# Kernel optimization log

Hardware: AMD Instinct MI355X
Metric: run time of the kernel (lower is better)

The kernel has to match this reference:

```python
import jax, jax.numpy as jnp
import numpy as np
from jax import lax

T, B, IN = 50, 1024, 405
H, NMEM, DMEM, R, NWAY = 200, 128, 40, 4, 5
GAMMA = 0.99


def setup_inputs() -> dict:
    key = jax.random.key(0)
    ks = jax.random.split(key, 11)
    s = lambda *sh: 0.05
    return {
        "x": jax.random.normal(ks[0], (T, B, IN), jnp.float32),
        "W_ih": jax.random.normal(ks[1], (4 * H, IN), jnp.float32) * 0.05,
        "W_hh": jax.random.normal(ks[2], (4 * H, H), jnp.float32) * 0.05,
        "b_ih": jax.random.normal(ks[3], (4 * H,), jnp.float32) * 0.05,
        "b_hh": jax.random.normal(ks[4], (4 * H,), jnp.float32) * 0.05,
        "Wk": jax.random.normal(ks[5], (R * DMEM, H), jnp.float32) * 0.05,
        "bk": jax.random.normal(ks[6], (R * DMEM,), jnp.float32) * 0.05,
        "Ws": jax.random.normal(ks[7], (R, H), jnp.float32) * 0.05,
        "bs": jax.random.normal(ks[8], (R,), jnp.float32) * 0.05,
        "Wo": jax.random.normal(ks[9], (NWAY, H + R * DMEM), jnp.float32) * 0.05,
        "bo": jax.random.normal(ks[10], (NWAY,), jnp.float32) * 0.05,
    }


def _ntm_forward(x, W_ih, W_hh, b_ih, b_hh, Wk, bk, Ws, bs, Wo, bo):
    sg = lax.stop_gradient
    batch_idx = jnp.arange(B)

    def step(carry, x_t):
        h, c, M, wr, wu, wlu = carry
        # LSTM cell (torch nn.LSTMCell gate order: i, f, g, o)
        gates = x_t @ W_ih.T + b_ih + h @ W_hh.T + b_hh
        i, f, g, o = jnp.split(gates, 4, axis=-1)
        c = jax.nn.sigmoid(f) * c + jax.nn.sigmoid(i) * jnp.tanh(g)
        h = jax.nn.sigmoid(o) * jnp.tanh(c)
        # zero out least-used memory row (data-level op in torch)
        idx = jnp.argmin(wu, axis=1)
        M = M.at[batch_idx, idx].set(0.0)
        # keys and interpolation gate
        k = jnp.tanh(h @ Wk.T + bk).reshape(B, R, DMEM)
        sigma = jax.nn.sigmoid(jnp.tanh(h @ Ws.T + bs)).reshape(B, R, 1)
        # write weights and memory write
        ww = sigma * wr + (1.0 - sigma) * wlu[:, None, :]  # [B,R,NMEM]
        M = M + jnp.einsum("brm,brd->bmd", ww, k)
        # cosine-similarity read addressing
        nk = jnp.linalg.norm(k, axis=2)   # [B,R]
        nM = jnp.linalg.norm(M, axis=2)   # [B,NMEM]
        K = jnp.einsum("brd,bmd->brm", k, M) / (nk[:, :, None] * nM[:, None, :])
        wr_new = jax.nn.softmax(K, axis=-1)  # softmax over memory slots
        r = jnp.einsum("brm,bmd->brd", wr_new, M).reshape(B, R * DMEM)
        # output head: Linear -> Sigmoid -> Softmax (as in torch source)
        logits = jnp.concatenate([h, r], axis=1) @ Wo.T + bo
        out = jax.nn.softmax(jax.nn.sigmoid(logits), axis=-1)
        # usage update (all detached in torch)
        wr_d = sg(wr_new)
        wu = GAMMA * wu + jnp.sum(wr_d + sg(ww), axis=1)
        kth = -lax.top_k(-wu, R)[0][:, -1]  # k-th smallest usage
        wlu = sg((wu <= kth[:, None]).astype(M.dtype))
        return (h, c, sg(M), wr_d, wu, wlu), out

    carry0 = (
        jnp.zeros((B, H), x.dtype),
        jnp.zeros((B, H), x.dtype),
        jnp.zeros((B, NMEM, DMEM), x.dtype),
        jnp.zeros((B, R, NMEM), x.dtype),
        jnp.zeros((B, NMEM), x.dtype),
        jnp.ones((B, NMEM), x.dtype),
    )
    _, y = lax.scan(step, carry0, x)
    return y  # [T, B, NWAY]


def reference(x, W_ih, W_hh, b_ih, b_hh, Wk, bk, Ws, bs, Wo, bo):
    return _ntm_forward(x, W_ih, W_hh, b_ih, b_hh, Wk, bk, Ws, bs, Wo, bo)
```

## Files before the change

kernel.cpp:

```cpp
#include <hip/hip_runtime.h>
#include <stdint.h>

#define TSTEPS 50
#define BATCH  1024
#define INDIM  405
#define KP     448
#define HDIM   200
#define G4H    800
#define NMEM   128
#define DMEM   40
#define DPAD   41
#define RH     4
#define RD     160
#define NWAY   5
#define GAMMA_ 0.99f
#define NG     4
#define WROWS  928

typedef __attribute__((ext_vector_type(8))) short short8;
typedef __attribute__((ext_vector_type(4))) float f32x4;

__device__ __forceinline__ float sigmoidf_(float x) {
    return 1.f / (1.f + __expf(-x));
}
__device__ __forceinline__ float ftanh(float x) {
    float e = __expf(2.f * x);
    return 1.f - 2.f / (e + 1.f);
}
__device__ __forceinline__ unsigned short f2bf(float f) {
    uint32_t u = __float_as_uint(f);
    uint32_t r = u + 0x7FFFu + ((u >> 16) & 1u);
    return (unsigned short)(r >> 16);
}
__device__ __forceinline__ float bf2f(unsigned short h) {
    return __uint_as_float(((uint32_t)h) << 16);
}

__global__ void transpose_weights(const float* __restrict__ W_hh,
                                  const float* __restrict__ Wk,
                                  float* __restrict__ WhhT,
                                  float* __restrict__ WkT) {
    int i = blockIdx.x * 256 + threadIdx.x;
    if (i < HDIM * G4H) {
        int j = i / G4H, o = i % G4H;
        WhhT[i] = W_hh[o * HDIM + j];
    } else if (i < HDIM * G4H + HDIM * RD) {
        int e = i - HDIM * G4H;
        int j = e / RD, rd = e % RD;
        WkT[e] = Wk[rd * HDIM + j];
    }
}

__global__ __launch_bounds__(256) void convert_A(const float* __restrict__ x,
                                                 unsigned short* __restrict__ Ahi,
                                                 unsigned short* __restrict__ Alo) {
    int c = blockIdx.x * 256 + threadIdx.x;
    int r = blockIdx.y;
    if (c >= KP) return;
    float v = (c < INDIM) ? x[(size_t)r * INDIM + c] : 0.f;
    unsigned short hi = f2bf(v);
    unsigned short lo = f2bf(v - bf2f(hi));
    size_t o = (size_t)r * KP + c;
    Ahi[o] = hi;
    Alo[o] = lo;
}

__global__ __launch_bounds__(256) void convert_W(const float* __restrict__ W_ih,
                                                 unsigned short* __restrict__ Wpk) {
    int c = blockIdx.x * 256 + threadIdx.x;
    int n = blockIdx.y;
    int sec = blockIdx.z;
    if (c >= KP) return;
    float v = (n < G4H && c < INDIM) ? W_ih[(size_t)n * INDIM + c] : 0.f;
    unsigned short hi = f2bf(v);
    size_t o = (size_t)sec * WROWS * KP + (size_t)n * KP + c;
    Wpk[o] = (sec == 0) ? hi : f2bf(v - bf2f(hi));
}

__global__ __launch_bounds__(256) void gx_gemm_mfma(
        const unsigned short* __restrict__ Ahi,
        const unsigned short* __restrict__ Alo,
        const unsigned short* __restrict__ Wpk,
        const float* __restrict__ b_ih, const float* __restrict__ b_hh,
        float* __restrict__ gx) {
    __shared__ unsigned short Alds[128 * 64];
    __shared__ unsigned short Blds[128 * 64];
    const int tid = threadIdx.x;
    const int wv = tid >> 6, ln = tid & 63;
    const int wr = wv >> 1, wc = wv & 1;
    const int n0 = blockIdx.x * 128;
    const int m0 = blockIdx.y * 128;

    f32x4 acc[4][4];
#pragma unroll
    for (int m = 0; m < 4; ++m)
#pragma unroll
        for (int n = 0; n < 4; ++n) acc[m][n] = (f32x4){0.f, 0.f, 0.f, 0.f};

    int erow[4], ecol[4];
#pragma unroll
    for (int i = 0; i < 4; ++i) {
        int e = (i * 4 + wv) * 512 + ln * 8;
        erow[i] = e >> 6;
        ecol[i] = e & 63;
    }

    const unsigned short* Whi = Wpk;
    const unsigned short* Wlo = Wpk + (size_t)WROWS * KP;

#pragma unroll 1
    for (int s = 0; s < 3; ++s) {
        const unsigned short* Ab = ((s == 2) ? Alo : Ahi) + (size_t)m0 * KP;
        const unsigned short* Bb = ((s == 1) ? Wlo : Whi) + (size_t)n0 * KP;

        short8 ar[4], br[4];
#pragma unroll
        for (int i = 0; i < 4; ++i) {
            ar[i] = *(const short8*)&Ab[(size_t)erow[i] * KP + ecol[i]];
            br[i] = *(const short8*)&Bb[(size_t)erow[i] * KP + ecol[i]];
        }

#pragma unroll 1
        for (int k0 = 0; k0 < KP; k0 += 64) {
            __syncthreads();
#pragma unroll
            for (int i = 0; i < 4; ++i) {
                int e = (i * 4 + wv) * 512 + ln * 8;
                *(short8*)&Alds[e] = ar[i];
                *(short8*)&Blds[e] = br[i];
            }
            __syncthreads();
            if (k0 + 64 < KP) {
#pragma unroll
                for (int i = 0; i < 4; ++i) {
                    ar[i] = *(const short8*)&Ab[(size_t)erow[i] * KP + k0 + 64 + ecol[i]];
                    br[i] = *(const short8*)&Bb[(size_t)erow[i] * KP + k0 + 64 + ecol[i]];
                }
            }
#pragma unroll
            for (int ks = 0; ks < 2; ++ks) {
                short8 af[4], bf[4];
                int kcol = ks * 32 + (ln >> 4) * 8;
#pragma unroll
                for (int m = 0; m < 4; ++m) {
                    int row = wr * 64 + m * 16 + (ln & 15);
                    af[m] = *(const short8*)&Alds[row * 64 + kcol];
                }
#pragma unroll
                for (int n = 0; n < 4; ++n) {
                    int row = wc * 64 + n * 16 + (ln & 15);
                    bf[n] = *(const short8*)&Blds[row * 64 + kcol];
                }
#pragma unroll
                for (int m = 0; m < 4; ++m)
#pragma unroll
                    for (int n = 0; n < 4; ++n)
                        acc[m][n] = __builtin_amdgcn_mfma_f32_16x16x32_bf16(
                            af[m], bf[n], acc[m][n], 0, 0, 0);
            }
        }
    }

#pragma unroll
    for (int n = 0; n < 4; ++n) {
        int col = n0 + wc * 64 + n * 16 + (ln & 15);
        if (col >= G4H) continue;
        float bias = b_ih[col] + b_hh[col];
#pragma unroll
        for (int m = 0; m < 4; ++m) {
#pragma unroll
            for (int j = 0; j < 4; ++j) {
                int row = m0 + wr * 64 + m * 16 + (ln >> 4) * 4 + j;
                gx[(size_t)row * G4H + col] = acc[m][n][j] + bias;
            }
        }
    }
}

__global__ __launch_bounds__(256) void gx_gemm(const float* __restrict__ x,
                                               const float* __restrict__ W_ih,
                                               const float* __restrict__ b_ih,
                                               const float* __restrict__ b_hh,
                                               float* __restrict__ gx) {
    const int BM = 128, BN = 80, BK = 16;
    __shared__ float As[BK][BM];
    __shared__ float Bs[BK][BN];
    int m0 = blockIdx.y * BM;
    int n0 = blockIdx.x * BN;
    int tid = threadIdx.x;
    int tm = tid >> 4, tn = tid & 15;
    float acc[8][5];
#pragma unroll
    for (int i = 0; i < 8; ++i)
#pragma unroll
        for (int j = 0; j < 5; ++j) acc[i][j] = 0.f;

    for (int k0 = 0; k0 < INDIM; k0 += BK) {
        {
            int row = tid >> 1, kk = (tid & 1) * 8;
            const float* ap = x + (size_t)(m0 + row) * INDIM + k0 + kk;
#pragma unroll
            for (int i = 0; i < 8; ++i)
                As[kk + i][row] = (k0 + kk + i < INDIM) ? ap[i] : 0.f;
        }
        if (tid < 160) {
            int col = tid >> 1, kk = (tid & 1) * 8;
            const float* bp = W_ih + (size_t)(n0 + col) * INDIM + k0 + kk;
#pragma unroll
            for (int i = 0; i < 8; ++i)
                Bs[kk + i][col] = (k0 + kk + i < INDIM) ? bp[i] : 0.f;
        }
        __syncthreads();
#pragma unroll
        for (int k = 0; k < BK; ++k) {
            float a[8], b[5];
#pragma unroll
            for (int i = 0; i < 8; ++i) a[i] = As[k][tm * 8 + i];
#pragma unroll
            for (int j = 0; j < 5; ++j) b[j] = Bs[k][tn * 5 + j];
#pragma unroll
            for (int i = 0; i < 8; ++i)
#pragma unroll
                for (int j = 0; j < 5; ++j) acc[i][j] += a[i] * b[j];
        }
        __syncthreads();
    }
#pragma unroll
    for (int j = 0; j < 5; ++j) {
        int n = n0 + tn * 5 + j;
        float bias = b_ih[n] + b_hh[n];
#pragma unroll
        for (int i = 0; i < 8; ++i) {
            int m = m0 + tm * 8 + i;
            gx[(size_t)m * G4H + n] = acc[i][j] + bias;
        }
    }
}

__global__ __launch_bounds__(1024) void ntm_scan(
        const float* __restrict__ gx,
        const float* __restrict__ WhhT,
        const float* __restrict__ WkT,
        const float* __restrict__ bk,
        const float* __restrict__ Wsm,
        const float* __restrict__ bs,
        const float* __restrict__ Wo,
        const float* __restrict__ bo,
        float* __restrict__ out) {
    __shared__ float sM[NG][NMEM][DPAD];
    __shared__ float sh[NG][HDIM];
    __shared__ float sgate[NG][G4H];
    __shared__ float spartK[NG][4][RD];
    __shared__ float spartS[NG][RH][4];
    __shared__ float swr[NG][RH][NMEM];
    __shared__ float sww[NG][RH][NMEM];
    __shared__ float sKs[NG][RH][NMEM];
    __shared__ float swu[NG][NMEM];
    __shared__ float swlu[NG][NMEM];
    __shared__ float sk[NG][RH][DMEM];
    __shared__ float sr[NG][RD];
    __shared__ float snk[NG][RH];
    __shared__ float ssig[NG][RH];
    __shared__ float snM[NG][NMEM];
    __shared__ float stmp[NG][NWAY];
    __shared__ int   sidx[NG];

    const int tid = threadIdx.x;
    const int b0  = blockIdx.x * NG;

    for (int e = tid; e < NG * NMEM * DPAD; e += 1024) ((float*)sM)[e] = 0.f;
    for (int e = tid; e < NG * HDIM; e += 1024) ((float*)sh)[e] = 0.f;
    for (int e = tid; e < NG * RH * NMEM; e += 1024) ((float*)swr)[e] = 0.f;
    for (int e = tid; e < NG * NMEM; e += 1024) { ((float*)swu)[e] = 0.f; ((float*)swlu)[e] = 1.f; }

    float c_reg = 0.f;
    float gxr0 = 0.f, gxr1 = 0.f, gxr2 = 0.f, gxr3 = 0.f;
    if (tid < G4H) {
        const float* gxp = gx + (size_t)b0 * G4H + tid;
        gxr0 = gxp[0]; gxr1 = gxp[G4H]; gxr2 = gxp[2 * G4H]; gxr3 = gxp[3 * G4H];
    }
    __syncthreads();

    for (int t = 0; t < TSTEPS; ++t) {
        if (tid < G4H) {
            const int o = tid;
            float acc0 = 0.f, acc1 = 0.f, acc2 = 0.f, acc3 = 0.f;
#pragma unroll 2
            for (int j = 0; j < HDIM; j += 4) {
                float4 h0 = *(const float4*)&sh[0][j];
                float4 h1 = *(const float4*)&sh[1][j];
                float4 h2 = *(const float4*)&sh[2][j];
                float4 h3 = *(const float4*)&sh[3][j];
                float w0 = WhhT[(j + 0) * G4H + o];
                float w1 = WhhT[(j + 1) * G4H + o];
                float w2 = WhhT[(j + 2) * G4H + o];
                float w3 = WhhT[(j + 3) * G4H + o];
                acc0 += w0 * h0.x + w1 * h0.y + w2 * h0.z + w3 * h0.w;
                acc1 += w0 * h1.x + w1 * h1.y + w2 * h1.z + w3 * h1.w;
                acc2 += w0 * h2.x + w1 * h2.y + w2 * h2.z + w3 * h2.w;
                acc3 += w0 * h3.x + w1 * h3.y + w2 * h3.z + w3 * h3.w;
            }
            sgate[0][o] = acc0 + gxr0;
            sgate[1][o] = acc1 + gxr1;
            sgate[2][o] = acc2 + gxr2;
            sgate[3][o] = acc3 + gxr3;
            if (t + 1 < TSTEPS) {
                const float* gxp = gx + ((size_t)(t + 1) * BATCH + b0) * G4H + o;
                gxr0 = gxp[0]; gxr1 = gxp[G4H]; gxr2 = gxp[2 * G4H]; gxr3 = gxp[3 * G4H];
            }
        }
        __syncthreads();

        if (tid < NG * HDIM) {
            int gg = tid / HDIM, j = tid - gg * HDIM;
            float ig = sigmoidf_(sgate[gg][j]);
            float fg = sigmoidf_(sgate[gg][j + HDIM]);
            float gv = ftanh(sgate[gg][j + 2 * HDIM]);
            float og = sigmoidf_(sgate[gg][j + 3 * HDIM]);
            c_reg = fg * c_reg + ig * gv;
            sh[gg][j] = og * ftanh(c_reg);
        }
        __syncthreads();

        if (tid < 640) {
            int col = tid % RD, c = tid / RD;
            int jb = 52 * c - ((c == 3) ? 4 : 0);
            int je = jb + ((c < 2) ? 52 : 48);
            float a0 = 0.f, a1 = 0.f, a2 = 0.f, a3 = 0.f;
            for (int j = jb; j < je; j += 4) {
                float4 h0 = *(const float4*)&sh[0][j];
                float4 h1 = *(const float4*)&sh[1][j];
                float4 h2 = *(const float4*)&sh[2][j];
                float4 h3 = *(const float4*)&sh[3][j];
                float w0 = WkT[(j + 0) * RD + col];
                float w1 = WkT[(j + 1) * RD + col];
                float w2 = WkT[(j + 2) * RD + col];
                float w3 = WkT[(j + 3) * RD + col];
                a0 += w0 * h0.x + w1 * h0.y + w2 * h0.z + w3 * h0.w;
                a1 += w0 * h1.x + w1 * h1.y + w2 * h1.z + w3 * h1.w;
                a2 += w0 * h2.x + w1 * h2.y + w2 * h2.z + w3 * h2.w;
                a3 += w0 * h3.x + w1 * h3.y + w2 * h3.z + w3 * h3.w;
            }
            spartK[0][c][col] = a0; spartK[1][c][col] = a1;
            spartK[2][c][col] = a2; spartK[3][c][col] = a3;
        } else if (tid < 704) {
            int v = tid - 640; int g = v >> 4, rc = v & 15, r = rc >> 2, c = rc & 3;
            float a = 0.f;
            for (int j = 50 * c; j < 50 * c + 50; ++j) a += sh[g][j] * Wsm[r * HDIM + j];
            spartS[g][r][c] = a;
        } else if (tid < 960) {
            int a = tid - 704; int g = a >> 6, ln = a & 63;
            float v0 = swu[g][ln], v1 = swu[g][ln + 64];
            bool p1 = (v1 < v0);
            float mv = p1 ? v1 : v0;
            int   mi = p1 ? ln + 64 : ln;
#pragma unroll
            for (int off = 32; off; off >>= 1) {
                float ov = __shfl_xor(mv, off);
                int   oi = __shfl_xor(mi, off);
                if (ov < mv || (ov == mv && oi < mi)) { mv = ov; mi = oi; }
            }
            if (ln == 0) sidx[g] = mi;
        }
        __syncthreads();

        if (tid < 640) {
            int g = tid / RD, col = tid % RD;
            float s = spartK[g][0][col] + spartK[g][1][col]
                    + spartK[g][2][col] + spartK[g][3][col] + bk[col];
            sk[g][col / DMEM][col % DMEM] = ftanh(s);
        } else if (tid < 656) {
            int v = tid - 640; int g = v >> 2, r = v & 3;
            float s = spartS[g][r][0] + spartS[g][r][1]
                    + spartS[g][r][2] + spartS[g][r][3] + bs[r];
            ssig[g][r] = sigmoidf_(ftanh(s));
        } else if (tid < 816) {
            int v = tid - 656; int g = v / DMEM, d = v % DMEM;
            sM[g][sidx[g]][d] = 0.f;
        }
        __syncthreads();

#pragma unroll
        for (int q = 0; q < 2; ++q) {
            int e = tid + q * 1024;
            int g = e >> 9, rm = e & 511, r = rm >> 7, m = rm & 127;
            sww[g][r][m] = ssig[g][r] * swr[g][r][m] + (1.f - ssig[g][r]) * swlu[g][m];
        }
        if (tid < 16) {
            int g = tid >> 2, r = tid & 3;
            float s = 0.f;
            for (int d = 0; d < DMEM; ++d) { float v = sk[g][r][d]; s += v * v; }
            snk[g][r] = sqrtf(s);
        }
        __syncthreads();

        {
            int g = tid >> 8, mh = tid & 255, m = mh >> 1, d0 = (mh & 1) * 20;
            float w0 = sww[g][0][m], w1 = sww[g][1][m], w2 = sww[g][2][m], w3 = sww[g][3][m];
            for (int d = d0; d < d0 + 20; ++d) {
                float add = w0 * sk[g][0][d] + w1 * sk[g][1][d]
                          + w2 * sk[g][2][d] + w3 * sk[g][3][d];
                sM[g][m][d] += add;
            }
        }
        __syncthreads();

        if (tid < 512) {
            int g = tid >> 7, m = tid & 127;
            float s = 0.f;
            for (int d = 0; d < DMEM; ++d) { float v = sM[g][m][d]; s += v * v; }
            snM[g][m] = sqrtf(s);
        }
        __syncthreads();

#pragma unroll
        for (int q = 0; q < 2; ++q) {
            int e = tid + q * 1024;
            int g = e >> 9, rm = e & 511, r = rm >> 7, m = rm & 127;
            float acc = 0.f;
            for (int d = 0; d < DMEM; ++d) acc += sk[g][r][d] * sM[g][m][d];
            sKs[g][r][m] = acc / (snk[g][r] * snM[g][m]);
        }
        __syncthreads();

        {
            int w = tid >> 6, ln = tid & 63, g = w >> 2, r = w & 3;
            float a = sKs[g][r][ln];
            float b = sKs[g][r][ln + 64];
            float mx = fmaxf(a, b);
#pragma unroll
            for (int off = 32; off; off >>= 1) mx = fmaxf(mx, __shfl_xor(mx, off));
            float ea = __expf(a - mx), eb = __expf(b - mx);
            float s = ea + eb;
#pragma unroll
            for (int off = 32; off; off >>= 1) s += __shfl_xor(s, off);
            float inv = 1.f / s;
            swr[g][r][ln]      = ea * inv;
            swr[g][r][ln + 64] = eb * inv;
        }
        __syncthreads();

        if (tid < 640) {
            int g = tid / RD, rd = tid % RD, r = rd / DMEM, d = rd % DMEM;
            float acc = 0.f;
            for (int m = 0; m < NMEM; ++m) acc += swr[g][r][m] * sM[g][m][d];
            sr[g][rd] = acc;
        } else {
            for (int e = tid - 640; e < 512; e += 384) {
                int g = e >> 7, m = e & 127;
                float wu = GAMMA_ * swu[g][m];
#pragma unroll
                for (int r = 0; r < RH; ++r) wu += swr[g][r][m] + sww[g][r][m];
                swu[g][m] = wu;
            }
        }
        __syncthreads();

        if (tid < 640) {
            int g = tid / RD, v = tid % RD, o = v >> 5, ln = v & 31;
            const float* wrow = Wo + o * (HDIM + RD);
            float acc = 0.f;
            for (int j = ln; j < HDIM; j += 32) acc += sh[g][j] * wrow[j];
            for (int d = ln; d < RD; d += 32) acc += sr[g][d] * wrow[HDIM + d];
#pragma unroll
            for (int off = 16; off; off >>= 1) acc += __shfl_xor(acc, off, 32);
            if (ln == 0) stmp[g][o] = acc + bo[o];
        } else if (tid < 896) {
            int a = tid - 640; int g = a >> 6, ln = a & 63;
            float o0 = swu[g][ln], o1 = swu[g][ln + 64];
            float v0 = o0, v1 = o1, kth = 0.f;
#pragma unroll
            for (int it = 0; it < RH; ++it) {
                bool p1 = (v1 < v0);
                float mv = p1 ? v1 : v0;
                int   mi = p1 ? ln + 64 : ln;
                for (int off = 32; off; off >>= 1) {
                    float ov = __shfl_xor(mv, off);
                    int   oi = __shfl_xor(mi, off);
                    if (ov < mv || (ov == mv && oi < mi)) { mv = ov; mi = oi; }
                }
                kth = mv;
                if (mi == ln) v0 = __builtin_inff();
                else if (mi == ln + 64) v1 = __builtin_inff();
            }
            swlu[g][ln]      = (o0 <= kth) ? 1.f : 0.f;
            swlu[g][ln + 64] = (o1 <= kth) ? 1.f : 0.f;
        }
        __syncthreads();

        if (tid < NG) {
            int g = tid;
            float v[NWAY], mx = -1e30f;
#pragma unroll
            for (int o = 0; o < NWAY; ++o) { v[o] = sigmoidf_(stmp[g][o]); mx = fmaxf(mx, v[o]); }
            float s = 0.f;
#pragma unroll
            for (int o = 0; o < NWAY; ++o) { v[o] = __expf(v[o] - mx); s += v[o]; }
            float inv = 1.f / s;
            float* op = out + ((size_t)t * BATCH + (b0 + g)) * NWAY;
#pragma unroll
            for (int o = 0; o < NWAY; ++o) op[o] = v[o] * inv;
        }
    }
}

extern "C" void kernel_launch(void* const* d_in, const int* in_sizes, int n_in,
                              void* d_out, int out_size, void* d_ws, size_t ws_size,
                              hipStream_t stream) {
    const float* x    = (const float*)d_in[0];
    const float* W_ih = (const float*)d_in[1];
    const float* W_hh = (const float*)d_in[2];
    const float* b_ih = (const float*)d_in[3];
    const float* b_hh = (const float*)d_in[4];
    const float* Wk   = (const float*)d_in[5];
    const float* bk   = (const float*)d_in[6];
    const float* Wsm  = (const float*)d_in[7];
    const float* bs   = (const float*)d_in[8];
    const float* Wo   = (const float*)d_in[9];
    const float* bo   = (const float*)d_in[10];
    float* out = (float*)d_out;

    const size_t gx_elems   = (size_t)TSTEPS * BATCH * G4H;
    const size_t whht_elems = (size_t)HDIM * G4H;
    const size_t wkt_elems  = (size_t)HDIM * RD;
    const size_t f32_elems  = gx_elems + whht_elems + wkt_elems;
    const size_t a_elems    = (size_t)TSTEPS * BATCH * KP;
    const size_t w_elems    = (size_t)2 * WROWS * KP;
    const size_t need_f32   = f32_elems * sizeof(float);
    const size_t need_mfma  = need_f32 + (2 * a_elems + w_elems) * sizeof(unsigned short);
    if (ws_size < need_f32) return;

    float* ws   = (float*)d_ws;
    float* gxb  = ws;
    float* WhhT = ws + gx_elems;
    float* WkT  = WhhT + whht_elems;

    int tr_elems = HDIM * G4H + HDIM * RD;
    transpose_weights<<<dim3((tr_elems + 255) / 256), dim3(256), 0, stream>>>(W_hh, Wk, WhhT, WkT);

    if (ws_size >= need_mfma) {
        unsigned short* Ahi = (unsigned short*)(WkT + wkt_elems);
        unsigned short* Alo = Ahi + a_elems;
        unsigned short* Wpk = Alo + a_elems;
        convert_A<<<dim3(2, TSTEPS * BATCH), dim3(256), 0, stream>>>(x, Ahi, Alo);
        convert_W<<<dim3(2, WROWS, 2), dim3(256), 0, stream>>>(W_ih, Wpk);
        gx_gemm_mfma<<<dim3(7, (TSTEPS * BATCH) / 128), dim3(256), 0, stream>>>(
            Ahi, Alo, Wpk, b_ih, b_hh, gxb);
    } else {
        gx_gemm<<<dim3(G4H / 80, (TSTEPS * BATCH) / 128), dim3(256), 0, stream>>>(
            x, W_ih, b_ih, b_hh, gxb);
    }

    ntm_scan<<<dim3(BATCH / NG), dim3(1024), 0, stream>>>(gxb, WhhT, WkT, bk, Wsm, bs, Wo, bo, out);
}
```

Measured before the change: 1.649 ms.

## Use bf16 MFMA with hi/lo split for recurrent and key GEMMs, fuse scan stages

Measured after the change: 1.672 ms. Within noise of the previous version (+1.4%).

```diff
diff --git a/kernel.cpp b/kernel.cpp
--- a/kernel.cpp
+++ b/kernel.cpp
@@ -5,11 +5,13 @@
 #define BATCH  1024
 #define INDIM  405
 #define KP     448
+#define KH     224
+#define HBS    232
 #define HDIM   200
 #define G4H    800
 #define NMEM   128
 #define DMEM   40
-#define DPAD   41
+#define DPAD   44
 #define RH     4
 #define RD     160
 #define NWAY   5
@@ -36,18 +38,20 @@
     return __uint_as_float(((uint32_t)h) << 16);
 }
 
-__global__ void transpose_weights(const float* __restrict__ W_hh,
-                                  const float* __restrict__ Wk,
-                                  float* __restrict__ WhhT,
-                                  float* __restrict__ WkT) {
+__global__ __launch_bounds__(256) void convert_rec(const float* __restrict__ W_hh,
+                                                   const float* __restrict__ Wk,
+                                                   unsigned short* __restrict__ Whh_bf,
+                                                   unsigned short* __restrict__ Wk_bf) {
     int i = blockIdx.x * 256 + threadIdx.x;
-    if (i < HDIM * G4H) {
-        int j = i / G4H, o = i % G4H;
-        WhhT[i] = W_hh[o * HDIM + j];
-    } else if (i < HDIM * G4H + HDIM * RD) {
-        int e = i - HDIM * G4H;
-        int j = e / RD, rd = e % RD;
-        WkT[e] = Wk[rd * HDIM + j];
+    const int whh_e = G4H * KH;
+    const int wk_e  = RD * KH;
+    if (i < whh_e) {
+        int o = i / KH, k = i % KH;
+        Whh_bf[i] = f2bf(k < HDIM ? W_hh[o * HDIM + k] : 0.f);
+    } else if (i < whh_e + wk_e) {
+        int e = i - whh_e;
+        int o = e / KH, k = e % KH;
+        Wk_bf[e] = f2bf(k < HDIM ? Wk[o * HDIM + k] : 0.f);
     }
 }
 
@@ -237,10 +241,10 @@
     }
 }
 
-__global__ __launch_bounds__(1024) void ntm_scan(
+__global__ __launch_bounds__(1024, 4) void ntm_scan(
         const float* __restrict__ gx,
-        const float* __restrict__ WhhT,
-        const float* __restrict__ WkT,
+        const unsigned short* __restrict__ Whh_bf,
+        const unsigned short* __restrict__ Wk_bf,
         const float* __restrict__ bk,
         const float* __restrict__ Wsm,
         const float* __restrict__ bs,
@@ -249,9 +253,9 @@
         float* __restrict__ out) {
     __shared__ float sM[NG][NMEM][DPAD];
     __shared__ float sh[NG][HDIM];
+    __shared__ unsigned short shbf_hi[16][HBS];
+    __shared__ unsigned short shbf_lo[16][HBS];
     __shared__ float sgate[NG][G4H];
-    __shared__ float spartK[NG][4][RD];
-    __shared__ float spartS[NG][RH][4];
     __shared__ float swr[NG][RH][NMEM];
     __shared__ float sww[NG][RH][NMEM];
     __shared__ float sKs[NG][RH][NMEM];
@@ -267,89 +271,99 @@
 
     const int tid = threadIdx.x;
     const int b0  = blockIdx.x * NG;
+    const int w   = tid >> 6, l = tid & 63;
+    const int lr  = l & 15, lc = l >> 4;
 
     for (int e = tid; e < NG * NMEM * DPAD; e += 1024) ((float*)sM)[e] = 0.f;
     for (int e = tid; e < NG * HDIM; e += 1024) ((float*)sh)[e] = 0.f;
+    for (int e = tid; e < 16 * HBS; e += 1024) { ((unsigned short*)shbf_hi)[e] = 0; ((unsigned short*)shbf_lo)[e] = 0; }
     for (int e = tid; e < NG * RH * NMEM; e += 1024) ((float*)swr)[e] = 0.f;
     for (int e = tid; e < NG * NMEM; e += 1024) { ((float*)swu)[e] = 0.f; ((float*)swlu)[e] = 1.f; }
 
     float c_reg = 0.f;
     float gxr0 = 0.f, gxr1 = 0.f, gxr2 = 0.f, gxr3 = 0.f;
+    int pg = 0, pj = 0;
     if (tid < G4H) {
-        const float* gxp = gx + (size_t)b0 * G4H + tid;
-        gxr0 = gxp[0]; gxr1 = gxp[G4H]; gxr2 = gxp[2 * G4H]; gxr3 = gxp[3 * G4H];
+        pg = tid / HDIM; pj = tid - pg * HDIM;
+        const float* gxp = gx + (size_t)(b0 + pg) * G4H + pj;
+        gxr0 = gxp[0]; gxr1 = gxp[HDIM]; gxr2 = gxp[2 * HDIM]; gxr3 = gxp[3 * HDIM];
     }
     __syncthreads();
 
     for (int t = 0; t < TSTEPS; ++t) {
+        {
+            short8 bh[7], bl[7];
+#pragma unroll
+            for (int kk = 0; kk < 7; ++kk) {
+                bh[kk] = *(const short8*)&shbf_hi[lr][kk * 32 + lc * 8];
+                bl[kk] = *(const short8*)&shbf_lo[lr][kk * 32 + lc * 8];
+            }
+            for (int tile = w; tile < 50; tile += 16) {
+                const unsigned short* ap = Whh_bf + (size_t)(tile * 16 + lr) * KH + lc * 8;
+                short8 af[7];
+#pragma unroll
+                for (int kk = 0; kk < 7; ++kk) af[kk] = *(const short8*)&ap[kk * 32];
+                f32x4 acc = (f32x4){0.f, 0.f, 0.f, 0.f};
+#pragma unroll
+                for (int kk = 0; kk < 7; ++kk)
+                    acc = __builtin_amdgcn_mfma_f32_16x16x32_bf16(af[kk], bh[kk], acc, 0, 0, 0);
+#pragma unroll
+                for (int kk = 0; kk < 7; ++kk)
+                    acc = __builtin_amdgcn_mfma_f32_16x16x32_bf16(af[kk], bl[kk], acc, 0, 0, 0);
+                if (lr < NG) {
+#pragma unroll
+                    for (int j = 0; j < 4; ++j)
+                        sgate[lr][tile * 16 + lc * 4 + j] = acc[j];
+                }
+            }
+        }
+        __syncthreads();
+
         if (tid < G4H) {
-            const int o = tid;
-            float acc0 = 0.f, acc1 = 0.f, acc2 = 0.f, acc3 = 0.f;
-#pragma unroll 2
-            for (int j = 0; j < HDIM; j += 4) {
-                float4 h0 = *(const float4*)&sh[0][j];
-                float4 h1 = *(const float4*)&sh[1][j];
-                float4 h2 = *(const float4*)&sh[2][j];
-                float4 h3 = *(const float4*)&sh[3][j];
-                float w0 = WhhT[(j + 0) * G4H + o];
-                float w1 = WhhT[(j + 1) * G4H + o];
-                float w2 = WhhT[(j + 2) * G4H + o];
-                float w3 = WhhT[(j + 3) * G4H + o];
-                acc0 += w0 * h0.x + w1 * h0.y + w2 * h0.z + w3 * h0.w;
-                acc1 += w0 * h1.x + w1 * h1.y + w2 * h1.z + w3 * h1.w;
-                acc2 += w0 * h2.x + w1 * h2.y + w2 * h2.z + w3 * h2.w;
-                acc3 += w0 * h3.x + w1 * h3.y + w2 * h3.z + w3 * h3.w;
-            }
-            sgate[0][o] = acc0 + gxr0;
-            sgate[1][o] = acc1 + gxr1;
-            sgate[2][o] = acc2 + gxr2;
-            sgate[3][o] = acc3 + gxr3;
+            float ig = sigmoidf_(sgate[pg][pj] + gxr0);
+            float fg = sigmoidf_(sgate[pg][pj + HDIM] + gxr1);
+            float gv = ftanh(sgate[pg][pj + 2 * HDIM] + gxr2);
+            float og = sigmoidf_(sgate[pg][pj + 3 * HDIM] + gxr3);
+            c_reg = fg * c_reg + ig * gv;
+            float h = og * ftanh(c_reg);
+            sh[pg][pj] = h;
+            unsigned short hi = f2bf(h);
+            shbf_hi[pg][pj] = hi;
+            shbf_lo[pg][pj] = f2bf(h - bf2f(hi));
             if (t + 1 < TSTEPS) {
-                const float* gxp = gx + ((size_t)(t + 1) * BATCH + b0) * G4H + o;
-                gxr0 = gxp[0]; gxr1 = gxp[G4H]; gxr2 = gxp[2 * G4H]; gxr3 = gxp[3 * G4H];
-            }
-        }
-        __syncthreads();
-
-        if (tid < NG * HDIM) {
-            int gg = tid / HDIM, j = tid - gg * HDIM;
-            float ig = sigmoidf_(sgate[gg][j]);
-            float fg = sigmoidf_(sgate[gg][j + HDIM]);
-            float gv = ftanh(sgate[gg][j + 2 * HDIM]);
-            float og = sigmoidf_(sgate[gg][j + 3 * HDIM]);
-            c_reg = fg * c_reg + ig * gv;
-            sh[gg][j] = og * ftanh(c_reg);
-        }
-        __syncthreads();
-
-        if (tid < 640) {
-            int col = tid % RD, c = tid / RD;
-            int jb = 52 * c - ((c == 3) ? 4 : 0);
-            int je = jb + ((c < 2) ? 52 : 48);
-            float a0 = 0.f, a1 = 0.f, a2 = 0.f, a3 = 0.f;
-            for (int j = jb; j < je; j += 4) {
-                float4 h0 = *(const float4*)&sh[0][j];
-                float4 h1 = *(const float4*)&sh[1][j];
-                float4 h2 = *(const float4*)&sh[2][j];
-                float4 h3 = *(const float4*)&sh[3][j];
-                float w0 = WkT[(j + 0) * RD + col];
-                float w1 = WkT[(j + 1) * RD + col];
-                float w2 = WkT[(j + 2) * RD + col];
-                float w3 = WkT[(j + 3) * RD + col];
-                a0 += w0 * h0.x + w1 * h0.y + w2 * h0.z + w3 * h0.w;
-                a1 += w0 * h1.x + w1 * h1.y + w2 * h1.z + w3 * h1.w;
-                a2 += w0 * h2.x + w1 * h2.y + w2 * h2.z + w3 * h2.w;
-                a3 += w0 * h3.x + w1 * h3.y + w2 * h3.z + w3 * h3.w;
-            }
-            spartK[0][c][col] = a0; spartK[1][c][col] = a1;
-            spartK[2][c][col] = a2; spartK[3][c][col] = a3;
-        } else if (tid < 704) {
-            int v = tid - 640; int g = v >> 4, rc = v & 15, r = rc >> 2, c = rc & 3;
-            float a = 0.f;
-            for (int j = 50 * c; j < 50 * c + 50; ++j) a += sh[g][j] * Wsm[r * HDIM + j];
-            spartS[g][r][c] = a;
-        } else if (tid < 960) {
-            int a = tid - 704; int g = a >> 6, ln = a & 63;
+                const float* gxp = gx + ((size_t)(t + 1) * BATCH + b0 + pg) * G4H + pj;
+                gxr0 = gxp[0]; gxr1 = gxp[HDIM]; gxr2 = gxp[2 * HDIM]; gxr3 = gxp[3 * HDIM];
+            }
+        }
+        __syncthreads();
+
+        if (w < 10) {
+            short8 bh[7], bl[7];
+#pragma unroll
+            for (int kk = 0; kk < 7; ++kk) {
+                bh[kk] = *(const short8*)&shbf_hi[lr][kk * 32 + lc * 8];
+                bl[kk] = *(const short8*)&shbf_lo[lr][kk * 32 + lc * 8];
+            }
+            const unsigned short* ap = Wk_bf + (size_t)(w * 16 + lr) * KH + lc * 8;
+            short8 af[7];
+#pragma unroll
+            for (int kk = 0; kk < 7; ++kk) af[kk] = *(const short8*)&ap[kk * 32];
+            f32x4 acc = (f32x4){0.f, 0.f, 0.f, 0.f};
+#pragma unroll
+            for (int kk = 0; kk < 7; ++kk)
+                acc = __builtin_amdgcn_mfma_f32_16x16x32_bf16(af[kk], bh[kk], acc, 0, 0, 0);
+#pragma unroll
+            for (int kk = 0; kk < 7; ++kk)
+                acc = __builtin_amdgcn_mfma_f32_16x16x32_bf16(af[kk], bl[kk], acc, 0, 0, 0);
+            if (lr < NG) {
+#pragma unroll
+                for (int j = 0; j < 4; ++j) {
+                    int o = w * 16 + lc * 4 + j;
+                    sk[lr][o / DMEM][o % DMEM] = ftanh(acc[j] + bk[o]);
+                }
+            }
+        } else if (tid < 896) {
+            int a = tid - 640; int g = a >> 6, ln = a & 63;
             float v0 = swu[g][ln], v1 = swu[g][ln + 64];
             bool p1 = (v1 < v0);
             float mv = p1 ? v1 : v0;
@@ -361,22 +375,59 @@
                 if (ov < mv || (ov == mv && oi < mi)) { mv = ov; mi = oi; }
             }
             if (ln == 0) sidx[g] = mi;
-        }
-        __syncthreads();
-
-        if (tid < 640) {
-            int g = tid / RD, col = tid % RD;
-            float s = spartK[g][0][col] + spartK[g][1][col]
-                    + spartK[g][2][col] + spartK[g][3][col] + bk[col];
-            sk[g][col / DMEM][col % DMEM] = ftanh(s);
-        } else if (tid < 656) {
-            int v = tid - 640; int g = v >> 2, r = v & 3;
-            float s = spartS[g][r][0] + spartS[g][r][1]
-                    + spartS[g][r][2] + spartS[g][r][3] + bs[r];
-            ssig[g][r] = sigmoidf_(ftanh(s));
-        } else if (tid < 816) {
-            int v = tid - 656; int g = v / DMEM, d = v % DMEM;
-            sM[g][sidx[g]][d] = 0.f;
+        } else {
+            int v = tid - 896;
+            int g = v >> 5, r = (v >> 3) & 3, cc = v & 7;
+            const float* wrow = Wsm + r * HDIM;
+            float p = 0.f;
+            for (int j = cc * 25; j < cc * 25 + 25; ++j) p += sh[g][j] * wrow[j];
+            p += __shfl_xor(p, 1);
+            p += __shfl_xor(p, 2);
+            p += __shfl_xor(p, 4);
+            if (cc == 0) ssig[g][r] = sigmoidf_(ftanh(p + bs[r]));
+        }
+        __syncthreads();
+
+        {
+            int g = tid >> 8, mh = tid & 255, m = mh >> 1, dh = mh & 1;
+            float sg0 = ssig[g][0], sg1 = ssig[g][1], sg2 = ssig[g][2], sg3 = ssig[g][3];
+            float wl = swlu[g][m];
+            float w0 = sg0 * swr[g][0][m] + (1.f - sg0) * wl;
+            float w1 = sg1 * swr[g][1][m] + (1.f - sg1) * wl;
+            float w2 = sg2 * swr[g][2][m] + (1.f - sg2) * wl;
+            float w3 = sg3 * swr[g][3][m] + (1.f - sg3) * wl;
+            if (!dh) {
+                sww[g][0][m] = w0; sww[g][1][m] = w1;
+                sww[g][2][m] = w2; sww[g][3][m] = w3;
+            }
+            bool zr = (m == sidx[g]);
+            int d0 = dh * 20;
+#pragma unroll
+            for (int q = 0; q < 5; ++q) {
+                int d = d0 + q * 4;
+                float4 mv = *(const float4*)&sM[g][m][d];
+                float4 k0 = *(const float4*)&sk[g][0][d];
+                float4 k1 = *(const float4*)&sk[g][1][d];
+                float4 k2 = *(const float4*)&sk[g][2][d];
+                float4 k3 = *(const float4*)&sk[g][3][d];
+                float4 o;
+                o.x = (zr ? 0.f : mv.x) + w0 * k0.x + w1 * k1.x + w2 * k2.x + w3 * k3.x;
+                o.y = (zr ? 0.f : mv.y) + w0 * k0.y + w1 * k1.y + w2 * k2.y + w3 * k3.y;
+                o.z = (zr ? 0.f : mv.z) + w0 * k0.z + w1 * k1.z + w2 * k2.z + w3 * k3.z;
+                o.w = (zr ? 0.f : mv.w) + w0 * k0.w + w1 * k1.w + w2 * k2.w + w3 * k3.w;
+                *(float4*)&sM[g][m][d] = o;
+            }
+            if (tid < 16) {
+                int g2 = tid >> 2, r2 = tid & 3;
+                float a0 = 0.f, a1 = 0.f, a2 = 0.f, a3 = 0.f;
+#pragma unroll
+                for (int q = 0; q < 10; ++q) {
+                    float4 kv = *(const float4*)&sk[g2][r2][q * 4];
+                    a0 += kv.x * kv.x; a1 += kv.y * kv.y;
+                    a2 += kv.z * kv.z; a3 += kv.w * kv.w;
+                }
+                snk[g2][r2] = sqrtf((a0 + a1) + (a2 + a3));
+            }
         }
         __syncthreads();
 
@@ -384,49 +435,34 @@
         for (int q = 0; q < 2; ++q) {
             int e = tid + q * 1024;
             int g = e >> 9, rm = e & 511, r = rm >> 7, m = rm & 127;
-            sww[g][r][m] = ssig[g][r] * swr[g][r][m] + (1.f - ssig[g][r]) * swlu[g][m];
-        }
-        if (tid < 16) {
-            int g = tid >> 2, r = tid & 3;
-            float s = 0.f;
-            for (int d = 0; d < DMEM; ++d) { float v = sk[g][r][d]; s += v * v; }
-            snk[g][r] = sqrtf(s);
-        }
-        __syncthreads();
-
-        {
-            int g = tid >> 8, mh = tid & 255, m = mh >> 1, d0 = (mh & 1) * 20;
-            float w0 = sww[g][0][m], w1 = sww[g][1][m], w2 = sww[g][2][m], w3 = sww[g][3][m];
-            for (int d = d0; d < d0 + 20; ++d) {
-                float add = w0 * sk[g][0][d] + w1 * sk[g][1][d]
-                          + w2 * sk[g][2][d] + w3 * sk[g][3][d];
-                sM[g][m][d] += add;
-            }
-        }
-        __syncthreads();
-
+            float a0 = 0.f, a1 = 0.f, a2 = 0.f, a3 = 0.f;
+#pragma unroll
+            for (int d4 = 0; d4 < 10; ++d4) {
+                float4 kv = *(const float4*)&sk[g][r][d4 * 4];
+                float4 mv = *(const float4*)&sM[g][m][d4 * 4];
+                a0 += kv.x * mv.x; a1 += kv.y * mv.y;
+                a2 += kv.z * mv.z; a3 += kv.w * mv.w;
+            }
+            sKs[g][r][m] = (a0 + a1) + (a2 + a3);
+        }
         if (tid < 512) {
             int g = tid >> 7, m = tid & 127;
-            float s = 0.f;
-            for (int d = 0; d < DMEM; ++d) { float v = sM[g][m][d]; s += v * v; }
-            snM[g][m] = sqrtf(s);
-        }
-        __syncthreads();
-
-#pragma unroll
-        for (int q = 0; q < 2; ++q) {
-            int e = tid + q * 1024;
-            int g = e >> 9, rm = e & 511, r = rm >> 7, m = rm & 127;
-            float acc = 0.f;
-            for (int d = 0; d < DMEM; ++d) acc += sk[g][r][d] * sM[g][m][d];
-            sKs[g][r][m] = acc / (snk[g][r] * snM[g][m]);
+            float a0 = 0.f, a1 = 0.f, a2 = 0.f, a3 = 0.f;
+#pragma unroll
+            for (int d4 = 0; d4 < 10; ++d4) {
+                float4 mv = *(const float4*)&sM[g][m][d4 * 4];
+                a0 += mv.x * mv.x; a1 += mv.y * mv.y;
+                a2 += mv.z * mv.z; a3 += mv.w * mv.w;
+            }
+            snM[g][m] = sqrtf((a0 + a1) + (a2 + a3));
         }
         __syncthreads();
 
         {
-            int w = tid >> 6, ln = tid & 63, g = w >> 2, r = w & 3;
-            float a = sKs[g][r][ln];
-            float b = sKs[g][r][ln + 64];
+            int g = w >> 2, r = w & 3, ln = l;
+            float ink = snk[g][r];
+            float a = sKs[g][r][ln] / (ink * snM[g][ln]);
+            float b = sKs[g][r][ln + 64] / (ink * snM[g][ln + 64]);
             float mx = fmaxf(a, b);
 #pragma unroll
             for (int off = 32; off; off >>= 1) mx = fmaxf(mx, __shfl_xor(mx, off));
@@ -440,12 +476,18 @@
         }
         __syncthreads();
 
-        if (tid < 640) {
-            int g = tid / RD, rd = tid % RD, r = rd / DMEM, d = rd % DMEM;
-            float acc = 0.f;
-            for (int m = 0; m < NMEM; ++m) acc += swr[g][r][m] * sM[g][m][d];
-            sr[g][rd] = acc;
-        } else {
+        if (tid < 160) {
+            int g = tid / 40, rd4 = tid % 40, r = rd4 / 10, d4 = rd4 % 10;
+            float a0 = 0.f, a1 = 0.f, a2 = 0.f, a3 = 0.f;
+            for (int m = 0; m < NMEM; ++m) {
+                float wv = swr[g][r][m];
+                float4 mv = *(const float4*)&sM[g][m][d4 * 4];
+                a0 += wv * mv.x; a1 += wv * mv.y;
+                a2 += wv * mv.z; a3 += wv * mv.w;
+            }
+            float4 res = {a0, a1, a2, a3};
+            *(float4*)&sr[g][r * DMEM + d4 * 4] = res;
+        } else if (tid >= 640) {
             for (int e = tid - 640; e < 512; e += 384) {
                 int g = e >> 7, m = e & 127;
                 float wu = GAMMA_ * swu[g][m];
@@ -520,26 +562,26 @@
     const float* bo   = (const float*)d_in[10];
     float* out = (float*)d_out;
 
-    const size_t gx_elems   = (size_t)TSTEPS * BATCH * G4H;
-    const size_t whht_elems = (size_t)HDIM * G4H;
-    const size_t wkt_elems  = (size_t)HDIM * RD;
-    const size_t f32_elems  = gx_elems + whht_elems + wkt_elems;
-    const size_t a_elems    = (size_t)TSTEPS * BATCH * KP;
-    const size_t w_elems    = (size_t)2 * WROWS * KP;
-    const size_t need_f32   = f32_elems * sizeof(float);
-    const size_t need_mfma  = need_f32 + (2 * a_elems + w_elems) * sizeof(unsigned short);
-    if (ws_size < need_f32) return;
-
-    float* ws   = (float*)d_ws;
-    float* gxb  = ws;
-    float* WhhT = ws + gx_elems;
-    float* WkT  = WhhT + whht_elems;
-
-    int tr_elems = HDIM * G4H + HDIM * RD;
-    transpose_weights<<<dim3((tr_elems + 255) / 256), dim3(256), 0, stream>>>(W_hh, Wk, WhhT, WkT);
+    const size_t gx_elems  = (size_t)TSTEPS * BATCH * G4H;
+    const size_t whh_e     = (size_t)G4H * KH;
+    const size_t wk_e      = (size_t)RD * KH;
+    const size_t a_elems   = (size_t)TSTEPS * BATCH * KP;
+    const size_t w_elems   = (size_t)2 * WROWS * KP;
+    const size_t need_base = gx_elems * 4 + (whh_e + wk_e) * 2;
+    const size_t need_mfma = need_base + (2 * a_elems + w_elems) * 2;
+    if (ws_size < need_base) return;
+
+    float* gxb = (float*)d_ws;
+    unsigned short* Whh_bf = (unsigned short*)(gxb + gx_elems);
+    unsigned short* Wk_bf  = Whh_bf + whh_e;
+
+    {
+        int tot = (int)(whh_e + wk_e);
+        convert_rec<<<dim3((tot + 255) / 256), dim3(256), 0, stream>>>(W_hh, Wk, Whh_bf, Wk_bf);
+    }
 
     if (ws_size >= need_mfma) {
-        unsigned short* Ahi = (unsigned short*)(WkT + wkt_elems);
+        unsigned short* Ahi = Wk_bf + wk_e;
         unsigned short* Alo = Ahi + a_elems;
         unsigned short* Wpk = Alo + a_elems;
         convert_A<<<dim3(2, TSTEPS * BATCH), dim3(256), 0, stream>>>(x, Ahi, Alo);
@@ -551,5 +593,6 @@
             x, W_ih, b_ih, b_hh, gxb);
     }
 
-    ntm_scan<<<dim3(BATCH / NG), dim3(1024), 0, stream>>>(gxb, WhhT, WkT, bk, Wsm, bs, Wo, bo, out);
-}
+    ntm_scan<<<dim3(BATCH / NG), dim3(1024), 0, stream>>>(
+        gxb, Whh_bf, Wk_bf, bk, Wsm, bs, Wo, bo, out);
+}
```
